# Optimization experiments

Hardware: AMD Instinct MI355X
Metric: run time of the kernel (lower is better)

Reference implementation:

```python
import jax, jax.numpy as jnp
import numpy as np

# plan steps: (downsample_factor, bins_min, bins_max)
PLAN = [(2, 10, 14), (4, 16, 20)]


def _downsample(x, scale):
    # F.interpolate(mode='linear', align_corners=False, scale_factor=1/scale)
    in_len = x.shape[-1]
    out_len = in_len // scale
    sf = in_len / out_len
    src = jnp.maximum((jnp.arange(out_len, dtype=jnp.float32) + 0.5) * sf - 0.5, 0.0)
    i0 = jnp.floor(src).astype(jnp.int32)
    w = src - i0
    i1 = jnp.minimum(i0 + 1, in_len - 1)
    return x[..., i0] * (1.0 - w) + x[..., i1] * w


def _groupshiftadd(x, g):
    # one FFA butterfly stage with group size g
    B, C, R, nc = x.shape
    xg = x.reshape(B, C, R // g, g, nc)
    i = np.arange(g)
    iA = i // 2
    iB = iA + g // 2
    Bs = (i + 1) // 2
    # roll(v, Bs): y[j] = v[(j - Bs) mod nc]; static gather indices
    col = (np.arange(nc)[None, :] - Bs[:, None]) % nc  # (g, nc)
    a = xg[:, :, :, iA, :]                     # (B,C,G,g,nc)
    b = xg[:, :, :, iB[:, None], col]          # (B,C,G,g,nc) shifted rows
    return (a + b).reshape(B, C, R, nc)


def _forward(x):
    std_dev = jnp.std(x, axis=2, ddof=1)  # torch .std(2) is unbiased
    outs = []
    for ds, bmin, bmax in PLAN:
        down = _downsample(x, ds)
        L = down.shape[-1]
        for bins in range(bmin, bmax):
            trunc = L % bins
            arr = down[:, :, :L - trunc] if trunc else down
            r = arr.reshape(arr.shape[0], arr.shape[1], -1, bins)
            ini_rows = r.shape[2]
            k = int(np.ceil(np.log2(ini_rows)))
            target_rows = 2 ** k
            add = target_rows - ini_rows
            if add:
                pad = jnp.zeros((r.shape[0], r.shape[1], add, bins), r.dtype)
                r = jnp.concatenate([r, pad], axis=2)
            y = r
            for stage in range(1, k + 1):
                y = _groupshiftadd(y, 2 ** stage)
            mx = y.max(axis=3)
            # torch.median returns lower middle element for even sizes
            med = jnp.sort(y, axis=3)[..., (bins - 1) // 2]
            snr = (mx - med) / std_dev[:, :, None] / np.sqrt(float(ini_rows))
            outs.append(snr)  # (B, C, target_rows)
    return jnp.concatenate(outs, axis=2)


def setup_inputs() -> dict:
    key = jax.random.key(0)
    x = jax.random.normal(key, (8, 4, 262144), dtype=jnp.float32)
    return {"x": x}


def reference(x):
    return _forward(x)
```

## Files before the change

kernel.cpp:

```cpp
#include <hip/hip_runtime.h>
#include <cmath>


constexpr int NSEQ    = 32;
constexpr int NLEN    = 262144;
constexpr int OUTROWS = 81920;
constexpr int STDCH   = 32;

constexpr int cilog2(int v) { int r = 0; while (v > 1) { v >>= 1; ++r; } return r; }

constexpr size_t SCROFF[8] = {0, 6291456, 12582912, 18874368,
                              27262976, 29360128, 31981568, 34603008};

template<int B>
__device__ __forceinline__ int mb(int x) { return ((x % B) + B) % B; }

__device__ __forceinline__ unsigned bf16rne(float f) {
    unsigned u = __float_as_uint(f);
    return (u + 0x7FFFu + ((u >> 16) & 1u)) >> 16;
}
__device__ __forceinline__ unsigned pk2(float lo, float hi) {
    return bf16rne(lo) | (bf16rne(hi) << 16);
}

__global__ __launch_bounds__(256)
void std_partial(const float* __restrict__ x, float2* __restrict__ part)
{
    const int seq = blockIdx.x, ch = blockIdx.y;
    constexpr int N4 = NLEN / 4 / STDCH;
    const float4* xp = reinterpret_cast<const float4*>(x + (size_t)seq * NLEN) + (size_t)ch * N4;
    float s = 0.f, s2 = 0.f;
    for (int i = threadIdx.x; i < N4; i += 256) {
        float4 v = xp[i];
        s  += (v.x + v.y) + (v.z + v.w);
        s2 += (v.x * v.x + v.y * v.y) + (v.z * v.z + v.w * v.w);
    }
    #pragma unroll
    for (int off = 32; off > 0; off >>= 1) {
        s  += __shfl_down(s, off, 64);
        s2 += __shfl_down(s2, off, 64);
    }
    __shared__ float2 ws[4];
    const int w = threadIdx.x >> 6, l = threadIdx.x & 63;
    if (l == 0) ws[w] = make_float2(s, s2);
    __syncthreads();
    if (threadIdx.x == 0) {
        float a = ws[0].x + ws[1].x + ws[2].x + ws[3].x;
        float b = ws[0].y + ws[1].y + ws[2].y + ws[3].y;
        part[seq * STDCH + ch] = make_float2(a, b);
    }
}

template<int BINS, int G, int H, int LQ>
__device__ __forceinline__
void fusedA(const float* __restrict__ src, float* __restrict__ dst, int s)
{
    constexpr int QUADS = G / 4;
    const int t = threadIdx.x;
    const int Q   = t & (QUADS - 1);
    const int chi = t >> LQ;
    const int c0  = chi * H;
    const int h = 1 << (s - 1), S = 1 << s;
    const int q  = Q & (h - 1);
    const int G2 = (Q >> (s - 1)) << (s + 1);
    const int rA0 = G2 + q, rA1 = rA0 + h, rB0 = G2 + S + q, rB1 = rB0 + h;
    const int vo = G2 + 4 * q;
    int ca = mb<BINS>(c0 - q), ga = mb<BINS>(c0 - 2 * q), cb = mb<BINS>(c0 - 3 * q);
    float a1p  = src[mb<BINS>(c0 - q - 1) * G + rA1];
    float b1p  = src[mb<BINS>(c0 - 3 * q - 1) * G + rB1];
    float b0m1 = src[mb<BINS>(c0 - 2 * q - 1) * G + rB0];
    float b0m2 = src[mb<BINS>(c0 - 2 * q - 2) * G + rB0];
    float b1m2 = src[mb<BINS>(c0 - 3 * q - 2) * G + rB1];
    float b1m3 = src[mb<BINS>(c0 - 3 * q - 3) * G + rB1];
    float v0p = b0m1 + b1p, v1p = b0m1 + b1m2, v1pp = b0m2 + b1m3;
    #pragma unroll
    for (int i2 = 0; i2 < H; ++i2) {
        const int c = c0 + i2;
        if (c < BINS) {
            float a0 = src[c * G + rA0];
            float a1 = src[ca * G + rA1];
            float b0 = src[ga * G + rB0];
            float b1 = src[cb * G + rB1];
            float u0 = a0 + a1, u1 = a0 + a1p;
            float v0 = b0 + b1, v1 = b0 + b1p;
            float4 o; o.x = u0 + v0; o.y = u0 + v0p; o.z = u1 + v1p; o.w = u1 + v1pp;
            *reinterpret_cast<float4*>(&dst[c * G + vo]) = o;
            a1p = a1; b1p = b1; v1pp = v1p; v1p = v1; v0p = v0;
            ++ca; if (ca == BINS) ca = 0;
            ++ga; if (ga == BINS) ga = 0;
            ++cb; if (cb == BINS) cb = 0;
        }
    }
}

template<int BINS, int G, int H, int LQ>
__device__ __forceinline__
void fusedA1(const float* __restrict__ src, float* __restrict__ dst)
{
    constexpr int QUADS = G / 4;
    const int t = threadIdx.x;
    const int Q   = t & (QUADS - 1);
    const int chi = t >> LQ;
    const int c0  = chi * H;
    const int r4  = 4 * Q;
    float4 fm1 = *reinterpret_cast<const float4*>(&src[mb<BINS>(c0 - 1) * G + r4]);
    float4 fm2 = *reinterpret_cast<const float4*>(&src[mb<BINS>(c0 - 2) * G + r4]);
    float4 fm3 = *reinterpret_cast<const float4*>(&src[mb<BINS>(c0 - 3) * G + r4]);
    float a1p = fm1.y, b1p = fm1.w;
    float v0p  = fm1.z + fm1.w;
    float v1p  = fm1.z + fm2.w;
    float v1pp = fm2.z + fm3.w;
    #pragma unroll
    for (int i2 = 0; i2 < H; ++i2) {
        const int c = c0 + i2;
        if (c < BINS) {
            float4 f = *reinterpret_cast<const float4*>(&src[c * G + r4]);
            float u0 = f.x + f.y, u1 = f.x + a1p;
            float v0 = f.z + f.w, v1 = f.z + b1p;
            float4 o; o.x = u0 + v0; o.y = u0 + v0p; o.z = u1 + v1p; o.w = u1 + v1pp;
            *reinterpret_cast<float4*>(&dst[c * G + r4]) = o;
            a1p = f.y; b1p = f.w; v1pp = v1p; v1p = v1; v0p = v0;
        }
    }
}

template<int BINS, int G, int H1, int LP>
__device__ __forceinline__
void singleA(const float* __restrict__ src, float* __restrict__ dst, int s)
{
    constexpr int PAIRS = G / 2;
    const int t = threadIdx.x;
    const int pr  = t & (PAIRS - 1);
    const int chi = t >> LP;
    const int c0  = chi * H1;
    const int half = 1 << (s - 1);
    const int qp = pr & (half - 1);
    const int grpbase = (pr >> (s - 1)) << s;
    const int rA = grpbase + qp, rB = rA + half, ro = grpbase + 2 * qp;
    const int shift = qp % BINS;
    int sc = mb<BINS>(c0 - shift);
    float bprev = src[mb<BINS>(c0 - shift - 1) * G + rB];
    #pragma unroll
    for (int i2 = 0; i2 < H1; ++i2) {
        const int c = c0 + i2;
        if (c < BINS) {
            float a  = src[c * G + rA];
            float bc = src[sc * G + rB];
            float2 o; o.x = a + bc; o.y = a + bprev;
            *reinterpret_cast<float2*>(&dst[c * G + ro]) = o;
            bprev = bc;
            ++sc; if (sc == BINS) sc = 0;
        }
    }
}

template<int DS, int BINS, int K, int S0, int CPAD>
__device__ __forceinline__
void passA_body(float* __restrict__ buf, const float* __restrict__ xs,
                unsigned short* __restrict__ scrC, int R, int blk, int sl)
{
    constexpr int G      = 1 << S0;
    constexpr int M      = 1 << (K - S0);
    constexpr int QUADS  = G / 4;
    constexpr int LQ     = cilog2(QUADS);
    constexpr int CSPLIT = 512 / QUADS;
    constexpr int H      = (BINS + CSPLIT - 1) / CSPLIT;
    constexpr int PAIRS  = G / 2;
    constexpr int LP     = cilog2(PAIRS);
    constexpr int CS1    = 512 / PAIRS;
    constexpr int H1     = (BINS + CS1 - 1) / CS1;
    const int t = threadIdx.x;
    float* b0 = buf;
    float* b1 = buf + BINS * G;

    const int fmax = max(0, min(G * BINS, R * BINS - blk * G * BINS));

    if constexpr (DS == 2) {
        const float4* src4 = reinterpret_cast<const float4*>(xs + 2 * (size_t)blk * G * BINS);
        constexpr int NF4 = G * BINS / 2;
        for (int i = t; i < NF4; i += 512) {
            const int f0 = 2 * i;
            if (f0 < fmax) {
                float4 v = src4[i];
                int lr = f0 / BINS, c = f0 - lr * BINS;
                b0[c * G + lr] = 0.5f * (v.x + v.y);
                if (f0 + 1 < fmax) {
                    int c1 = c + 1, lr1 = lr;
                    if (c1 == BINS) { c1 = 0; ++lr1; }
                    b0[c1 * G + lr1] = 0.5f * (v.z + v.w);
                }
            }
        }
    } else {
        const float4* src4 = reinterpret_cast<const float4*>(xs + 4 * (size_t)blk * G * BINS);
        constexpr int NF4 = G * BINS;
        for (int i = t; i < NF4; i += 512) {
            if (i < fmax) {
                float4 v = src4[i];
                int lr = i / BINS, c = i - lr * BINS;
                b0[c * G + lr] = 0.5f * (v.y + v.z);
            }
        }
    }
    for (int f = fmax + t; f < G * BINS; f += 512) {
        int lr = f / BINS, c = f - lr * BINS;
        b0[c * G + lr] = 0.f;
    }
    __syncthreads();

    fusedA1<BINS, G, H, LQ>(b0, b1);    __syncthreads();
    fusedA <BINS, G, H, LQ>(b1, b0, 3); __syncthreads();
    fusedA <BINS, G, H, LQ>(b0, b1, 5); __syncthreads();
    fusedA <BINS, G, H, LQ>(b1, b0, 7); __syncthreads();
    if constexpr (S0 == 9) {
        singleA<BINS, G, H1, LP>(b0, b1, 9); __syncthreads();
    }

    const float* fin = (S0 & 1) ? b1 : b0;
    if constexpr (G == 512) {
        const int lr = t;
        unsigned u[CPAD / 2];
        #pragma unroll
        for (int k = 0; k < CPAD / 2; ++k) {
            const int ca = 2 * k, cbn = 2 * k + 1;
            float fa = (ca < BINS)  ? fin[ca * G + lr]  : 0.f;
            float fb = (cbn < BINS) ? fin[cbn * G + lr] : 0.f;
            u[k] = pk2(fa, fb);
        }
        unsigned short* dst = scrC + ((size_t)(sl * M + blk) * G + lr) * CPAD;
        if constexpr (CPAD == 12) {
            uint2* d2 = reinterpret_cast<uint2*>(dst);
            d2[0] = make_uint2(u[0], u[1]);
            d2[1] = make_uint2(u[2], u[3]);
            d2[2] = make_uint2(u[4], u[5]);
        } else {
            uint4* d4 = reinterpret_cast<uint4*>(dst);
            d4[0] = make_uint4(u[0], u[1], u[2], u[3]);
            d4[1] = make_uint4(u[4], u[5], u[6], u[7]);
        }
    } else {
        const int lr = t & 255, chh = t >> 8;
        constexpr int CH = CPAD / 2;
        unsigned u[CH / 2];
        #pragma unroll
        for (int k = 0; k < CH / 2; ++k) {
            const int ca = chh * CH + 2 * k, cbn = ca + 1;
            float fa = (ca < BINS)  ? fin[ca * G + lr]  : 0.f;
            float fb = (cbn < BINS) ? fin[cbn * G + lr] : 0.f;
            u[k] = pk2(fa, fb);
        }
        unsigned short* dst = scrC + ((size_t)(sl * M + blk) * G + lr) * CPAD + chh * CH;
        if constexpr (CH == 8) {
            *reinterpret_cast<uint4*>(dst) = make_uint4(u[0], u[1], u[2], u[3]);
        } else {
            unsigned* d = reinterpret_cast<unsigned*>(dst);
            #pragma unroll
            for (int k = 0; k < CH / 2; ++k) d[k] = u[k];
        }
    }
}

__global__ __launch_bounds__(512, 6)
void passA_all(const float* __restrict__ x, unsigned short* __restrict__ scr)
{
    __shared__ float buf[2 * 13 * 512];
    const int b = blockIdx.x;
    if (b < 4096) {
        const int cfg = b >> 10, r = b & 1023, blk = r & 31, sl = r >> 5;
        const float* xs = x + (size_t)sl * NLEN;
        switch (cfg) {
            case 0: passA_body<2, 10, 14, 9, 12>(buf, xs, scr + SCROFF[0], 13107, blk, sl); break;
            case 1: passA_body<2, 11, 14, 9, 12>(buf, xs, scr + SCROFF[1], 11915, blk, sl); break;
            case 2: passA_body<2, 12, 14, 9, 12>(buf, xs, scr + SCROFF[2], 10922, blk, sl); break;
            default: passA_body<2, 13, 14, 9, 16>(buf, xs, scr + SCROFF[3], 10082, blk, sl); break;
        }
    } else {
        const int b2 = b - 4096;
        const int cfg = b2 >> 9, r = b2 & 511, blk = r & 15, sl = r >> 4;
        const float* xs = x + (size_t)sl * NLEN;
        switch (cfg) {
            case 0: passA_body<4, 16, 12, 8, 16>(buf, xs, scr + SCROFF[4], 4096, blk, sl); break;
            case 1: passA_body<4, 17, 12, 8, 20>(buf, xs, scr + SCROFF[5], 3855, blk, sl); break;
            case 2: passA_body<4, 18, 12, 8, 20>(buf, xs, scr + SCROFF[6], 3640, blk, sl); break;
            default: passA_body<4, 19, 12, 8, 20>(buf, xs, scr + SCROFF[7], 3449, blk, sl); break;
        }
    }
}

template<int BINS, int M, int CST, int HB, int LQ>
__device__ __forceinline__
void fusedB(float* __restrict__ zpg, int s, int p, int sub)
{
    constexpr int QUADS = M / 4;
    const int Q   = sub & (QUADS - 1);
    const int chi = sub >> LQ;
    const int c0  = chi * HB;
    const int h = 1 << (s - 1), S = 1 << s;
    const int q  = Q & (h - 1);
    const int G2 = (Q >> (s - 1)) << (s + 1);
    const int rA0 = G2 + q, rA1 = rA0 + h, rB0 = G2 + S + q, rB1 = rB0 + h;
    const int vo = G2 + 4 * q;
    const int ba1 = mb<BINS>(c0 - q - p * h - 1);
    const int bb0 = mb<BINS>(c0 - 2 * q - p * S - 2);
    const int bb1 = mb<BINS>(c0 - 3 * q - p * (S + h) - 3);

    float fa0[HB], fa1[HB + 1], fb0[HB + 2], fb1[HB + 3];
    #pragma unroll
    for (int i = 0; i < HB; ++i) {
        int cc = c0 + i; if (cc >= BINS) cc = BINS - 1;
        fa0[i] = zpg[cc * CST + rA0];
    }
    int idx = ba1;
    #pragma unroll
    for (int i = 0; i < HB + 1; ++i) {
        fa1[i] = zpg[idx * CST + rA1];
        ++idx; if (idx == BINS) idx = 0;
    }
    idx = bb0;
    #pragma unroll
    for (int i = 0; i < HB + 2; ++i) {
        fb0[i] = zpg[idx * CST + rB0];
        ++idx; if (idx == BINS) idx = 0;
    }
    idx = bb1;
    #pragma unroll
    for (int i = 0; i < HB + 3; ++i) {
        fb1[i] = zpg[idx * CST + rB1];
        ++idx; if (idx == BINS) idx = 0;
    }
    __syncthreads();
    #pragma unroll
    for (int i2 = 0; i2 < HB; ++i2) {
        const int c = c0 + i2;
        if (c < BINS) {
            float u0 = fa0[i2] + fa1[i2 + 1];
            float u1 = fa0[i2] + fa1[i2];
            float v0c  = fb0[i2 + 2] + fb1[i2 + 3];
            float v0p  = fb0[i2 + 1] + fb1[i2 + 2];
            float v1p  = fb0[i2 + 1] + fb1[i2 + 1];
            float v1pp = fb0[i2]     + fb1[i2];
            float4 o; o.x = u0 + v0c; o.y = u0 + v0p; o.z = u1 + v1p; o.w = u1 + v1pp;
            *reinterpret_cast<float4*>(&zpg[c * CST + vo]) = o;
        }
    }
    __syncthreads();
}

template<int BINS, int M, int CST, int HSB, int LP>
__device__ __forceinline__
void singleB(float* __restrict__ zpg, int s, int p, int sub)
{
    constexpr int PAIRSB = M / 2;
    const int pr  = sub & (PAIRSB - 1);
    const int chi = sub >> LP;
    const int c0  = chi * HSB;
    const int half = 1 << (s - 1);
    const int qp = pr & (half - 1);
    const int grpbase = (pr >> (s - 1)) << s;
    const int rA = grpbase + qp, rB = rA + half, ro = grpbase + 2 * qp;
    const int shift = (qp + p * half) % BINS;

    float ra[HSB], rb[HSB + 1];
    #pragma unroll
    for (int i = 0; i < HSB; ++i) {
        int cc = c0 + i; if (cc >= BINS) cc = BINS - 1;
        ra[i] = zpg[cc * CST + rA];
    }
    int idx = mb<BINS>(c0 - shift - 1);
    #pragma unroll
    for (int i = 0; i < HSB + 1; ++i) {
        rb[i] = zpg[idx * CST + rB];
        ++idx; if (idx == BINS) idx = 0;
    }
    __syncthreads();
    #pragma unroll
    for (int i2 = 0; i2 < HSB; ++i2) {
        const int c = c0 + i2;
        if (c < BINS) {
            float2 o; o.x = ra[i2] + rb[i2 + 1]; o.y = ra[i2] + rb[i2];
            *reinterpret_cast<float2*>(&zpg[c * CST + ro]) = o;
        }
    }
    __syncthreads();
}

template<int BINS, int K, int S0, int CPAD, int OUTOFF>
__device__ __forceinline__
void passB_body(float* __restrict__ zb, float* __restrict__ s_red,
                const unsigned short* __restrict__ scrC, const float2* __restrict__ part,
                float* __restrict__ out, int R, int p_base, int sl)
{
    constexpr int G    = 1 << S0;
    constexpr int M    = 1 << (K - S0);
    constexpr int TS   = K - S0;
    constexpr int P    = 16;
    constexpr int CST  = M + 4;
    constexpr int BCST = BINS * CST;
    constexpr int LQB  = cilog2(M / 4);
    constexpr int CHB  = 32 / (M / 4);
    constexpr int HB   = (BINS + CHB - 1) / CHB;
    constexpr int LPB  = cilog2(M / 2);
    constexpr int CSB  = 32 / (M / 2);
    constexpr int HSB  = (BINS + CSB - 1) / CSB;

    const int t = threadIdx.x;

    if (t < 64) {
        float s = 0.f, s2 = 0.f;
        if (t < 32) { float2 pp = part[sl * STDCH + t]; s = pp.x; s2 = pp.y; }
        #pragma unroll
        for (int off = 16; off > 0; off >>= 1) {
            s  += __shfl_down(s, off, 64);
            s2 += __shfl_down(s2, off, 64);
        }
        if (t == 0) {
            const float n = (float)NLEN;
            s_red[0] = rsqrtf((s2 - s * s / n) / (n - 1.f)) * rsqrtf((float)R);
        }
    }

    {
        constexpr int RUN = P * CPAD / 4;
        constexpr int TOT = M * RUN;
        const unsigned short* base = scrC + (size_t)sl * M * G * CPAD + (size_t)p_base * CPAD;
        for (int i = t; i < TOT; i += 512) {
            const int v = i / RUN, r = i - v * RUN;
            const uint2 d = *reinterpret_cast<const uint2*>(base + (size_t)v * G * CPAD + 4 * r);
            const int e0 = 4 * r;
            const int pl = e0 / CPAD, c = e0 - pl * CPAD;
            float* zp = zb + pl * BCST + v;
            if (c + 0 < BINS) zp[(c + 0) * CST] = __uint_as_float(d.x << 16);
            if (c + 1 < BINS) zp[(c + 1) * CST] = __uint_as_float(d.x & 0xFFFF0000u);
            if (c + 2 < BINS) zp[(c + 2) * CST] = __uint_as_float(d.y << 16);
            if (c + 3 < BINS) zp[(c + 3) * CST] = __uint_as_float(d.y & 0xFFFF0000u);
        }
    }
    __syncthreads();

    const int sub = t & 31, pg = t >> 5;
    const int p = p_base + pg;
    float* zpg = zb + pg * BCST;
    fusedB<BINS, M, CST, HB, LQB>(zpg, 1, p, sub);
    fusedB<BINS, M, CST, HB, LQB>(zpg, 3, p, sub);
    if constexpr (TS == 5) {
        singleB<BINS, M, CST, HSB, LPB>(zpg, 5, p, sub);
    }

    constexpr int ROWS = P * M;
    if (t < ROWS) {
        const int pg2 = t >> TS;
        const int v   = t & (M - 1);
        const float* z = zb + pg2 * BCST;
        float a[BINS];
        #pragma unroll
        for (int c = 0; c < BINS; ++c) a[c] = z[c * CST + v];
        float mx = a[0];
        #pragma unroll
        for (int c = 1; c < BINS; ++c) mx = fmaxf(mx, a[c]);
        constexpr int MIDX = (BINS - 1) / 2;
        #pragma unroll
        for (int i = 0; i <= MIDX; ++i) {
            #pragma unroll
            for (int j = i + 1; j < BINS; ++j) {
                float lo = fminf(a[i], a[j]);
                float hi = fmaxf(a[i], a[j]);
                a[i] = lo; a[j] = hi;
            }
        }
        out[(size_t)sl * OUTROWS + OUTOFF + (size_t)p_base * M + t] = (mx - a[MIDX]) * s_red[0];
    }
}

__global__ __launch_bounds__(512, 6)
void passB_all(const unsigned short* __restrict__ scr, const float2* __restrict__ part,
               float* __restrict__ out)
{
    __shared__ float zb[16 * 13 * 36];
    __shared__ float s_red[1];
    const int b = blockIdx.x;
    if (b < 4096) {
        const int cfg = b >> 10, r = b & 1023, pb = r & 31, sl = r >> 5;
        const int p_base = pb * 16;
        switch (cfg) {
            case 0: passB_body<10, 14, 9, 12, 0>    (zb, s_red, scr + SCROFF[0], part, out, 13107, p_base, sl); break;
            case 1: passB_body<11, 14, 9, 12, 16384>(zb, s_red, scr + SCROFF[1], part, out, 11915, p_base, sl); break;
            case 2: passB_body<12, 14, 9, 12, 32768>(zb, s_red, scr + SCROFF[2], part, out, 10922, p_base, sl); break;
            default: passB_body<13, 14, 9, 16, 49152>(zb, s_red, scr + SCROFF[3], part, out, 10082, p_base, sl); break;
        }
    } else {
        const int b2 = b - 4096;
        const int cfg = b2 >> 9, r = b2 & 511, pb = r & 15, sl = r >> 4;
        const int p_base = pb * 16;
        switch (cfg) {
            case 0: passB_body<16, 12, 8, 16, 65536>(zb, s_red, scr + SCROFF[4], part, out, 4096, p_base, sl); break;
            case 1: passB_body<17, 12, 8, 20, 69632>(zb, s_red, scr + SCROFF[5], part, out, 3855, p_base, sl); break;
            case 2: passB_body<18, 12, 8, 20, 73728>(zb, s_red, scr + SCROFF[6], part, out, 3640, p_base, sl); break;
            default: passB_body<19, 12, 8, 20, 77824>(zb, s_red, scr + SCROFF[7], part, out, 3449, p_base, sl); break;
        }
    }
}

extern "C" void kernel_launch(void* const* d_in, const int* in_sizes, int n_in,
                              void* d_out, int out_size, void* d_ws, size_t ws_size,
                              hipStream_t stream)
{
    (void)in_sizes; (void)n_in; (void)out_size; (void)ws_size;
    const float* x = (const float*)d_in[0];
    float* out  = (float*)d_out;
    float* wsf  = (float*)d_ws;
    float2* part = reinterpret_cast<float2*>(wsf + 64);
    unsigned short* scr = reinterpret_cast<unsigned short*>(wsf + 2176);

    hipLaunchKernelGGL(std_partial, dim3(NSEQ, STDCH), dim3(256), 0, stream, x, part);
    hipLaunchKernelGGL(passA_all, dim3(6144), dim3(512), 0, stream, x, scr);
    hipLaunchKernelGGL(passB_all, dim3(6144), dim3(512), 0, stream, scr, part, out);
}
```

Measured before the change: 162.7 us.

## Replace ping-pong radix-4 passA stages with in-place radix-2 stages in padded LDS

The passA butterfly stages drop the double-buffered LDS scheme with fused two-stage (quad) updates. Instead, each stage is done in place in one padded buffer (stride G+4): a thread loads its values into registers, syncs, then writes back. This halves shared memory per block, and the launch bound is raised from 6 to 8 blocks per CU to gain occupancy. The cost is more stages and barriers (S0 radix-2 passes instead of four fused passes plus one), so LDS traffic rises. The modulo helper is also replaced with inline wraparound code.

```diff
diff --git a/kernel.cpp b/kernel.cpp
--- a/kernel.cpp
+++ b/kernel.cpp
@@ -11,9 +11,6 @@
 
 constexpr size_t SCROFF[8] = {0, 6291456, 12582912, 18874368,
                               27262976, 29360128, 31981568, 34603008};
-
-template<int B>
-__device__ __forceinline__ int mb(int x) { return ((x % B) + B) % B; }
 
 __device__ __forceinline__ unsigned bf16rne(float f) {
     unsigned u = __float_as_uint(f);
@@ -51,83 +48,11 @@
     }
 }
 
-template<int BINS, int G, int H, int LQ>
-__device__ __forceinline__
-void fusedA(const float* __restrict__ src, float* __restrict__ dst, int s)
-{
-    constexpr int QUADS = G / 4;
-    const int t = threadIdx.x;
-    const int Q   = t & (QUADS - 1);
-    const int chi = t >> LQ;
-    const int c0  = chi * H;
-    const int h = 1 << (s - 1), S = 1 << s;
-    const int q  = Q & (h - 1);
-    const int G2 = (Q >> (s - 1)) << (s + 1);
-    const int rA0 = G2 + q, rA1 = rA0 + h, rB0 = G2 + S + q, rB1 = rB0 + h;
-    const int vo = G2 + 4 * q;
-    int ca = mb<BINS>(c0 - q), ga = mb<BINS>(c0 - 2 * q), cb = mb<BINS>(c0 - 3 * q);
-    float a1p  = src[mb<BINS>(c0 - q - 1) * G + rA1];
-    float b1p  = src[mb<BINS>(c0 - 3 * q - 1) * G + rB1];
-    float b0m1 = src[mb<BINS>(c0 - 2 * q - 1) * G + rB0];
-    float b0m2 = src[mb<BINS>(c0 - 2 * q - 2) * G + rB0];
-    float b1m2 = src[mb<BINS>(c0 - 3 * q - 2) * G + rB1];
-    float b1m3 = src[mb<BINS>(c0 - 3 * q - 3) * G + rB1];
-    float v0p = b0m1 + b1p, v1p = b0m1 + b1m2, v1pp = b0m2 + b1m3;
-    #pragma unroll
-    for (int i2 = 0; i2 < H; ++i2) {
-        const int c = c0 + i2;
-        if (c < BINS) {
-            float a0 = src[c * G + rA0];
-            float a1 = src[ca * G + rA1];
-            float b0 = src[ga * G + rB0];
-            float b1 = src[cb * G + rB1];
-            float u0 = a0 + a1, u1 = a0 + a1p;
-            float v0 = b0 + b1, v1 = b0 + b1p;
-            float4 o; o.x = u0 + v0; o.y = u0 + v0p; o.z = u1 + v1p; o.w = u1 + v1pp;
-            *reinterpret_cast<float4*>(&dst[c * G + vo]) = o;
-            a1p = a1; b1p = b1; v1pp = v1p; v1p = v1; v0p = v0;
-            ++ca; if (ca == BINS) ca = 0;
-            ++ga; if (ga == BINS) ga = 0;
-            ++cb; if (cb == BINS) cb = 0;
-        }
-    }
-}
-
-template<int BINS, int G, int H, int LQ>
-__device__ __forceinline__
-void fusedA1(const float* __restrict__ src, float* __restrict__ dst)
-{
-    constexpr int QUADS = G / 4;
-    const int t = threadIdx.x;
-    const int Q   = t & (QUADS - 1);
-    const int chi = t >> LQ;
-    const int c0  = chi * H;
-    const int r4  = 4 * Q;
-    float4 fm1 = *reinterpret_cast<const float4*>(&src[mb<BINS>(c0 - 1) * G + r4]);
-    float4 fm2 = *reinterpret_cast<const float4*>(&src[mb<BINS>(c0 - 2) * G + r4]);
-    float4 fm3 = *reinterpret_cast<const float4*>(&src[mb<BINS>(c0 - 3) * G + r4]);
-    float a1p = fm1.y, b1p = fm1.w;
-    float v0p  = fm1.z + fm1.w;
-    float v1p  = fm1.z + fm2.w;
-    float v1pp = fm2.z + fm3.w;
-    #pragma unroll
-    for (int i2 = 0; i2 < H; ++i2) {
-        const int c = c0 + i2;
-        if (c < BINS) {
-            float4 f = *reinterpret_cast<const float4*>(&src[c * G + r4]);
-            float u0 = f.x + f.y, u1 = f.x + a1p;
-            float v0 = f.z + f.w, v1 = f.z + b1p;
-            float4 o; o.x = u0 + v0; o.y = u0 + v0p; o.z = u1 + v1p; o.w = u1 + v1pp;
-            *reinterpret_cast<float4*>(&dst[c * G + r4]) = o;
-            a1p = f.y; b1p = f.w; v1pp = v1p; v1p = v1; v0p = v0;
-        }
-    }
-}
-
 template<int BINS, int G, int H1, int LP>
 __device__ __forceinline__
-void singleA(const float* __restrict__ src, float* __restrict__ dst, int s)
-{
+void stageIP(float* __restrict__ buf, int s)
+{
+    constexpr int CST = G + 4;
     constexpr int PAIRS = G / 2;
     const int t = threadIdx.x;
     const int pr  = t & (PAIRS - 1);
@@ -138,20 +63,29 @@
     const int grpbase = (pr >> (s - 1)) << s;
     const int rA = grpbase + qp, rB = rA + half, ro = grpbase + 2 * qp;
     const int shift = qp % BINS;
-    int sc = mb<BINS>(c0 - shift);
-    float bprev = src[mb<BINS>(c0 - shift - 1) * G + rB];
-    #pragma unroll
-    for (int i2 = 0; i2 < H1; ++i2) {
-        const int c = c0 + i2;
+
+    float ra[H1], rb[H1 + 1];
+    #pragma unroll
+    for (int i = 0; i < H1; ++i) {
+        int cc = c0 + i; if (cc >= BINS) cc = BINS - 1;
+        ra[i] = buf[cc * CST + rA];
+    }
+    int idx = c0 - shift - 1; if (idx < 0) idx += BINS;
+    #pragma unroll
+    for (int i = 0; i < H1 + 1; ++i) {
+        rb[i] = buf[idx * CST + rB];
+        ++idx; if (idx == BINS) idx = 0;
+    }
+    __syncthreads();
+    #pragma unroll
+    for (int i = 0; i < H1; ++i) {
+        const int c = c0 + i;
         if (c < BINS) {
-            float a  = src[c * G + rA];
-            float bc = src[sc * G + rB];
-            float2 o; o.x = a + bc; o.y = a + bprev;
-            *reinterpret_cast<float2*>(&dst[c * G + ro]) = o;
-            bprev = bc;
-            ++sc; if (sc == BINS) sc = 0;
-        }
-    }
+            float2 o; o.x = ra[i] + rb[i + 1]; o.y = ra[i] + rb[i];
+            *reinterpret_cast<float2*>(&buf[c * CST + ro]) = o;
+        }
+    }
+    __syncthreads();
 }
 
 template<int DS, int BINS, int K, int S0, int CPAD>
@@ -159,19 +93,14 @@
 void passA_body(float* __restrict__ buf, const float* __restrict__ xs,
                 unsigned short* __restrict__ scrC, int R, int blk, int sl)
 {
-    constexpr int G      = 1 << S0;
-    constexpr int M      = 1 << (K - S0);
-    constexpr int QUADS  = G / 4;
-    constexpr int LQ     = cilog2(QUADS);
-    constexpr int CSPLIT = 512 / QUADS;
-    constexpr int H      = (BINS + CSPLIT - 1) / CSPLIT;
-    constexpr int PAIRS  = G / 2;
-    constexpr int LP     = cilog2(PAIRS);
-    constexpr int CS1    = 512 / PAIRS;
-    constexpr int H1     = (BINS + CS1 - 1) / CS1;
+    constexpr int G     = 1 << S0;
+    constexpr int M     = 1 << (K - S0);
+    constexpr int CST   = G + 4;
+    constexpr int PAIRS = G / 2;
+    constexpr int LP    = cilog2(PAIRS);
+    constexpr int CS1   = 512 / PAIRS;
+    constexpr int H1    = (BINS + CS1 - 1) / CS1;
     const int t = threadIdx.x;
-    float* b0 = buf;
-    float* b1 = buf + BINS * G;
 
     const int fmax = max(0, min(G * BINS, R * BINS - blk * G * BINS));
 
@@ -183,11 +112,11 @@
             if (f0 < fmax) {
                 float4 v = src4[i];
                 int lr = f0 / BINS, c = f0 - lr * BINS;
-                b0[c * G + lr] = 0.5f * (v.x + v.y);
+                buf[c * CST + lr] = 0.5f * (v.x + v.y);
                 if (f0 + 1 < fmax) {
                     int c1 = c + 1, lr1 = lr;
                     if (c1 == BINS) { c1 = 0; ++lr1; }
-                    b0[c1 * G + lr1] = 0.5f * (v.z + v.w);
+                    buf[c1 * CST + lr1] = 0.5f * (v.z + v.w);
                 }
             }
         }
@@ -198,33 +127,28 @@
             if (i < fmax) {
                 float4 v = src4[i];
                 int lr = i / BINS, c = i - lr * BINS;
-                b0[c * G + lr] = 0.5f * (v.y + v.z);
+                buf[c * CST + lr] = 0.5f * (v.y + v.z);
             }
         }
     }
     for (int f = fmax + t; f < G * BINS; f += 512) {
         int lr = f / BINS, c = f - lr * BINS;
-        b0[c * G + lr] = 0.f;
-    }
-    __syncthreads();
-
-    fusedA1<BINS, G, H, LQ>(b0, b1);    __syncthreads();
-    fusedA <BINS, G, H, LQ>(b1, b0, 3); __syncthreads();
-    fusedA <BINS, G, H, LQ>(b0, b1, 5); __syncthreads();
-    fusedA <BINS, G, H, LQ>(b1, b0, 7); __syncthreads();
-    if constexpr (S0 == 9) {
-        singleA<BINS, G, H1, LP>(b0, b1, 9); __syncthreads();
-    }
-
-    const float* fin = (S0 & 1) ? b1 : b0;
+        buf[c * CST + lr] = 0.f;
+    }
+    __syncthreads();
+
+    for (int s = 1; s <= S0; ++s)
+        stageIP<BINS, G, H1, LP>(buf, s);
+
+    const float* fin = buf;
     if constexpr (G == 512) {
         const int lr = t;
         unsigned u[CPAD / 2];
         #pragma unroll
         for (int k = 0; k < CPAD / 2; ++k) {
             const int ca = 2 * k, cbn = 2 * k + 1;
-            float fa = (ca < BINS)  ? fin[ca * G + lr]  : 0.f;
-            float fb = (cbn < BINS) ? fin[cbn * G + lr] : 0.f;
+            float fa = (ca < BINS)  ? fin[ca * CST + lr]  : 0.f;
+            float fb = (cbn < BINS) ? fin[cbn * CST + lr] : 0.f;
             u[k] = pk2(fa, fb);
         }
         unsigned short* dst = scrC + ((size_t)(sl * M + blk) * G + lr) * CPAD;
@@ -245,8 +169,8 @@
         #pragma unroll
         for (int k = 0; k < CH / 2; ++k) {
             const int ca = chh * CH + 2 * k, cbn = ca + 1;
-            float fa = (ca < BINS)  ? fin[ca * G + lr]  : 0.f;
-            float fb = (cbn < BINS) ? fin[cbn * G + lr] : 0.f;
+            float fa = (ca < BINS)  ? fin[ca * CST + lr]  : 0.f;
+            float fb = (cbn < BINS) ? fin[cbn * CST + lr] : 0.f;
             u[k] = pk2(fa, fb);
         }
         unsigned short* dst = scrC + ((size_t)(sl * M + blk) * G + lr) * CPAD + chh * CH;
@@ -260,10 +184,10 @@
     }
 }
 
-__global__ __launch_bounds__(512, 6)
+__global__ __launch_bounds__(512, 8)
 void passA_all(const float* __restrict__ x, unsigned short* __restrict__ scr)
 {
-    __shared__ float buf[2 * 13 * 512];
+    __shared__ float buf[13 * 516];
     const int b = blockIdx.x;
     if (b < 4096) {
         const int cfg = b >> 10, r = b & 1023, blk = r & 31, sl = r >> 5;
@@ -300,9 +224,10 @@
     const int G2 = (Q >> (s - 1)) << (s + 1);
     const int rA0 = G2 + q, rA1 = rA0 + h, rB0 = G2 + S + q, rB1 = rB0 + h;
     const int vo = G2 + 4 * q;
-    const int ba1 = mb<BINS>(c0 - q - p * h - 1);
-    const int bb0 = mb<BINS>(c0 - 2 * q - p * S - 2);
-    const int bb1 = mb<BINS>(c0 - 3 * q - p * (S + h) - 3);
+    auto mbf = [](int x, int B) { int r = x % B; return r < 0 ? r + B : r; };
+    const int ba1 = mbf(c0 - q - p * h - 1, BINS);
+    const int bb0 = mbf(c0 - 2 * q - p * S - 2, BINS);
+    const int bb1 = mbf(c0 - 3 * q - p * (S + h) - 3, BINS);
 
     float fa0[HB], fa1[HB + 1], fb0[HB + 2], fb1[HB + 3];
     #pragma unroll
@@ -366,7 +291,8 @@
         int cc = c0 + i; if (cc >= BINS) cc = BINS - 1;
         ra[i] = zpg[cc * CST + rA];
     }
-    int idx = mb<BINS>(c0 - shift - 1);
+    int idx = c0 - shift - 1;
+    idx %= BINS; if (idx < 0) idx += BINS;
     #pragma unroll
     for (int i = 0; i < HSB + 1; ++i) {
         rb[i] = zpg[idx * CST + rB];
```

New measurement: 156.6 us. 1.04x faster.
